# Kernel tuning notes

Measured on AMD Instinct MI355X. Metric: run time of the kernel, lower is better.

Reference implementation:

```python
import jax, jax.numpy as jnp
import numpy as np

RANK = 16
ALPHA = 32.0
LORA_SCALE = ALPHA / RANK  # 2.0


def setup_inputs() -> dict:
    key = jax.random.key(0)
    ks = jax.random.split(key, 7)
    B_, S, D_IN, D_OUT = 4, 2048, 4096, 4096
    x = jax.random.normal(ks[0], (B_, S, D_IN), dtype=jnp.float32)
    qweight = jax.random.randint(ks[1], (D_OUT, D_IN), 0, 16, dtype=jnp.int32)
    w_min = jax.random.normal(ks[2], (D_OUT, 1), dtype=jnp.float32) * 0.1
    # row scale ~ (max-min)/15 of typical weights; keep positive
    w_scale = jax.random.uniform(ks[3], (D_OUT, 1), dtype=jnp.float32, minval=1e-3, maxval=0.02)
    bias = jax.random.normal(ks[4], (D_OUT,), dtype=jnp.float32) * 0.02
    A = jax.random.normal(ks[5], (RANK, D_IN), dtype=jnp.float32) * 0.02
    # module inits B to zeros; use small randn so the LoRA branch is exercised
    Bm = jax.random.normal(ks[6], (D_OUT, RANK), dtype=jnp.float32) * 0.02
    return {"x": x, "qweight": qweight, "w_min": w_min, "w_scale": w_scale,
            "bias": bias, "A": A, "B": Bm}


def reference(x, qweight, w_min, w_scale, bias, A, B):
    # Row-wise 4-bit dequant: W[o,i] = q[o,i]*scale[o] + min[o]
    base_weight = qweight.astype(jnp.float32) * w_scale + w_min  # [O, I]
    base_out = jnp.einsum('bsi,oi->bso', x, base_weight) + bias   # [B, S, O]
    # LoRA: (x @ A^T) @ B^T * (alpha/rank); dropout p=0 is identity
    lora_out = jnp.einsum('bsr,or->bso', jnp.einsum('bsi,ri->bsr', x, A), B) * LORA_SCALE
    return base_out + lora_out
```

## Files before the change

kernel.cpp:

```cpp
#include <hip/hip_runtime.h>
#include <hip/hip_bf16.h>

typedef unsigned short u16;
typedef unsigned int u32;
typedef __bf16 bf16x8 __attribute__((ext_vector_type(8)));
typedef float f32x4 __attribute__((ext_vector_type(4)));
typedef u16 u16x4 __attribute__((ext_vector_type(4)));
typedef u16 u16x8 __attribute__((ext_vector_type(8)));

#define D_IN 4096
#define D_OUT 4096
#define M_TOT 8192
#define RANK_ 16

#define BM 256
#define BN 256
#define BK 64
#define NT (D_IN / BK)
#define OPB 2

__device__ __forceinline__ u16 f2bf(float f) {
    union { float f; u32 u; } v; v.f = f;
    u32 u = v.u;
    u32 r = (u + 0x7FFFu + ((u >> 16) & 1u)) >> 16;
    return (u16)r;
}

__global__ __launch_bounds__(256) void dequant_fold_kernel(
        const int* __restrict__ q, const float* __restrict__ wmin,
        const float* __restrict__ wscale, const float* __restrict__ A,
        const float* __restrict__ Bm, u16* __restrict__ Wb) {
    const int K = D_IN;
    int o0 = blockIdx.x * OPB;
    float s0 = wscale[o0], s1 = wscale[o0 + 1];
    float m0 = wmin[o0],   m1 = wmin[o0 + 1];
    float Br0[RANK_], Br1[RANK_];
    #pragma unroll
    for (int r = 0; r < RANK_; ++r) {
        Br0[r] = 2.0f * Bm[(size_t)o0 * RANK_ + r];
        Br1[r] = 2.0f * Bm[(size_t)(o0 + 1) * RANK_ + r];
    }
    for (int i4 = threadIdx.x; i4 < K / 4; i4 += 256) {
        int i = i4 * 4;
        int4 q0 = *(const int4*)(q + (size_t)o0 * K + i);
        int4 q1 = *(const int4*)(q + (size_t)(o0 + 1) * K + i);
        float v00 = (float)q0.x * s0 + m0, v01 = (float)q0.y * s0 + m0;
        float v02 = (float)q0.z * s0 + m0, v03 = (float)q0.w * s0 + m0;
        float v10 = (float)q1.x * s1 + m1, v11 = (float)q1.y * s1 + m1;
        float v12 = (float)q1.z * s1 + m1, v13 = (float)q1.w * s1 + m1;
        #pragma unroll
        for (int r = 0; r < RANK_; ++r) {
            float4 av = *(const float4*)(A + (size_t)r * K + i);
            v00 += Br0[r] * av.x; v01 += Br0[r] * av.y;
            v02 += Br0[r] * av.z; v03 += Br0[r] * av.w;
            v10 += Br1[r] * av.x; v11 += Br1[r] * av.y;
            v12 += Br1[r] * av.z; v13 += Br1[r] * av.w;
        }
        u16x4 o0v, o1v;
        o0v.x = f2bf(v00); o0v.y = f2bf(v01); o0v.z = f2bf(v02); o0v.w = f2bf(v03);
        o1v.x = f2bf(v10); o1v.y = f2bf(v11); o1v.z = f2bf(v12); o1v.w = f2bf(v13);
        *(u16x4*)(Wb + (size_t)o0 * K + i) = o0v;
        *(u16x4*)(Wb + (size_t)(o0 + 1) * K + i) = o1v;
    }
}

__global__ void xcast_kernel(const float* __restrict__ x, u16* __restrict__ xb) {
    size_t i = (size_t)blockIdx.x * blockDim.x + threadIdx.x;
    const float4* p = (const float4*)x + i * 2;
    float4 a = p[0];
    float4 b = p[1];
    u16x8 o;
    o[0] = f2bf(a.x); o[1] = f2bf(a.y); o[2] = f2bf(a.z); o[3] = f2bf(a.w);
    o[4] = f2bf(b.x); o[5] = f2bf(b.y); o[6] = f2bf(b.z); o[7] = f2bf(b.w);
    *(u16x8*)(xb + i * 8) = o;
}


#define STAGE_R(sarr, larr, base, kt) do { _Pragma("unroll") \
    for (int j_ = 0; j_ < 2; ++j_) \
        __builtin_amdgcn_global_load_lds( \
            (__attribute__((address_space(1))) u32*)(sarr[j_] + (kt) * 64), \
            (__attribute__((address_space(3))) u32*)(smem + (base) + larr[j_]), \
            16, 0, 0); } while (0)

#define MFMA(d, va, vb) d = __builtin_amdgcn_mfma_f32_16x16x32_bf16(va, vb, d, 0, 0, 0)

__global__ __launch_bounds__(512, 2) void gemm_bt_kernel(const u16* __restrict__ Xb,
                                                         const u16* __restrict__ Wb,
                                                         const float* __restrict__ bias,
                                                         float* __restrict__ out) {
    extern __shared__ __align__(16) char smem[];
    const int K = D_IN, N = D_OUT;

    int bid = blockIdx.x;
    int swz = (bid & 7) * 64 + (bid >> 3);
    int tM = swz >> 4;
    int tN = swz & 15;

    int t = threadIdx.x;
    int lane = t & 63;
    int wave = t >> 6;
    int wm = wave >> 2;
    int wn = wave & 3;
    int lr = lane & 15;
    int hi = lane >> 4;
    int l7 = lane & 7;

    int xs0 = ((0 * 4 + hi) ^ l7) << 4;
    int xs1 = ((1 * 4 + hi) ^ l7) << 4;
    int aRow = (wm * 128 + lr) * 128;
    int bRow = (wn * 64 + lr) * 128;

    const u16 *srcA03[2], *srcA47[2], *srcB01[2], *srcB23[2];
    int ldsA03[2], ldsA47[2], ldsB01[2], ldsB23[2];
    #pragma unroll
    for (int j = 0; j < 2; ++j) {
        int idx = j * 512 + t;
        int rl = idx >> 3, slot = idx & 7;
        int rA = (rl & 63) + ((rl >> 6) << 7);
        int rB = (rl & 31) + ((rl >> 5) << 6);
        int r = rA;
        ldsA03[j] = r * 128 + slot * 16;
        srcA03[j] = Xb + (size_t)(tM * 256 + r) * K + ((slot ^ (r & 7)) << 3);
        r = rA + 64;
        ldsA47[j] = r * 128 + slot * 16;
        srcA47[j] = Xb + (size_t)(tM * 256 + r) * K + ((slot ^ (r & 7)) << 3);
        r = rB;
        ldsB01[j] = r * 128 + slot * 16;
        srcB01[j] = Wb + (size_t)(tN * 256 + r) * K + ((slot ^ (r & 7)) << 3);
        r = rB + 32;
        ldsB23[j] = r * 128 + slot * 16;
        srcB23[j] = Wb + (size_t)(tN * 256 + r) * K + ((slot ^ (r & 7)) << 3);
    }

    f32x4 acc[8][4];
    #pragma unroll
    for (int i = 0; i < 8; ++i)
        #pragma unroll
        for (int j = 0; j < 4; ++j)
            acc[i][j] = (f32x4){0.f, 0.f, 0.f, 0.f};

    STAGE_R(srcA03, ldsA03, 0, 0);     STAGE_R(srcA47, ldsA47, 0, 0);
    STAGE_R(srcB01, ldsB01, 65536, 0); STAGE_R(srcB23, ldsB23, 65536, 0);
    STAGE_R(srcA03, ldsA03, 32768, 1); STAGE_R(srcA47, ldsA47, 32768, 1);
    STAGE_R(srcB01, ldsB01, 98304, 1); STAGE_R(srcB23, ldsB23, 98304, 1);
    asm volatile("s_waitcnt vmcnt(8)" ::: "memory");
    __builtin_amdgcn_s_barrier();

    bf16x8 a[4][2], b23[2][2], b01[2][2];
    #pragma unroll
    for (int nf = 0; nf < 2; ++nf) {
        b01[nf][0] = *(const bf16x8*)(smem + 65536 + bRow + nf * 2048 + xs0);
        b01[nf][1] = *(const bf16x8*)(smem + 65536 + bRow + nf * 2048 + xs1);
    }

    for (int tt = 0; tt < NT; ++tt) {
        int pA = (tt & 1) * 32768;
        int pB = 65536 + (tt & 1) * 32768;
        int pBn = 65536 + ((~tt) & 1) * 32768;
        bool pre = (tt + 2 < NT);

        #pragma unroll
        for (int mf = 0; mf < 4; ++mf) {
            a[mf][0] = *(const bf16x8*)(smem + pA + aRow + mf * 2048 + xs0);
            a[mf][1] = *(const bf16x8*)(smem + pA + aRow + mf * 2048 + xs1);
        }
        asm volatile("s_waitcnt lgkmcnt(4)" ::: "memory");
        __builtin_amdgcn_s_barrier();
        asm volatile("s_waitcnt lgkmcnt(0)");
        __builtin_amdgcn_s_setprio(1);
        #pragma unroll
        for (int mf = 0; mf < 4; ++mf)
            #pragma unroll
            for (int nf = 0; nf < 2; ++nf) {
                MFMA(acc[mf][nf], a[mf][0], b01[nf][0]);
                MFMA(acc[mf][nf], a[mf][1], b01[nf][1]);
            }
        __builtin_amdgcn_s_setprio(0);
        __builtin_amdgcn_s_barrier();

        #pragma unroll
        for (int nf = 0; nf < 2; ++nf) {
            b23[nf][0] = *(const bf16x8*)(smem + pB + bRow + (nf + 2) * 2048 + xs0);
            b23[nf][1] = *(const bf16x8*)(smem + pB + bRow + (nf + 2) * 2048 + xs1);
        }
        if (pre) {
            STAGE_R(srcA03, ldsA03, pA, tt + 2);
            STAGE_R(srcB01, ldsB01, pB, tt + 2);
        }
        __builtin_amdgcn_s_barrier();
        asm volatile("s_waitcnt lgkmcnt(0)");
        __builtin_amdgcn_s_setprio(1);
        #pragma unroll
        for (int mf = 0; mf < 4; ++mf)
            #pragma unroll
            for (int nf = 0; nf < 2; ++nf) {
                MFMA(acc[mf][nf + 2], a[mf][0], b23[nf][0]);
                MFMA(acc[mf][nf + 2], a[mf][1], b23[nf][1]);
            }
        __builtin_amdgcn_s_setprio(0);
        __builtin_amdgcn_s_barrier();

        #pragma unroll
        for (int mf = 0; mf < 4; ++mf) {
            a[mf][0] = *(const bf16x8*)(smem + pA + aRow + (mf + 4) * 2048 + xs0);
            a[mf][1] = *(const bf16x8*)(smem + pA + aRow + (mf + 4) * 2048 + xs1);
        }
        if (pre) { STAGE_R(srcB23, ldsB23, pB, tt + 2); }
        asm volatile("s_waitcnt lgkmcnt(4)" ::: "memory");
        __builtin_amdgcn_s_barrier();
        asm volatile("s_waitcnt lgkmcnt(0)");
        __builtin_amdgcn_s_setprio(1);
        #pragma unroll
        for (int mf = 0; mf < 4; ++mf)
            #pragma unroll
            for (int nf = 0; nf < 2; ++nf) {
                MFMA(acc[mf + 4][nf], a[mf][0], b01[nf][0]);
                MFMA(acc[mf + 4][nf], a[mf][1], b01[nf][1]);
            }
        __builtin_amdgcn_s_setprio(0);
        __builtin_amdgcn_s_barrier();

        if (pre) { STAGE_R(srcA47, ldsA47, pA, tt + 2); }
        if (tt < NT - 2) { asm volatile("s_waitcnt vmcnt(8)" ::: "memory"); }
        else             { asm volatile("s_waitcnt vmcnt(0)" ::: "memory"); }
        __builtin_amdgcn_s_barrier();
        if (tt + 1 < NT) {
            #pragma unroll
            for (int nf = 0; nf < 2; ++nf) {
                b01[nf][0] = *(const bf16x8*)(smem + pBn + bRow + nf * 2048 + xs0);
                b01[nf][1] = *(const bf16x8*)(smem + pBn + bRow + nf * 2048 + xs1);
            }
        }
        __builtin_amdgcn_s_setprio(1);
        #pragma unroll
        for (int mf = 0; mf < 4; ++mf)
            #pragma unroll
            for (int nf = 0; nf < 2; ++nf) {
                MFMA(acc[mf + 4][nf + 2], a[mf][0], b23[nf][0]);
                MFMA(acc[mf + 4][nf + 2], a[mf][1], b23[nf][1]);
            }
        __builtin_amdgcn_s_setprio(0);
        __builtin_amdgcn_s_barrier();
    }

    #pragma unroll
    for (int nf = 0; nf < 4; ++nf) {
        int gn = tN * 256 + wn * 64 + nf * 16 + lr;
        float bs = bias[gn];
        #pragma unroll
        for (int mf = 0; mf < 8; ++mf) {
            #pragma unroll
            for (int r = 0; r < 4; ++r) {
                int gm = tM * 256 + wm * 128 + mf * 16 + hi * 4 + r;
                out[(size_t)gm * N + gn] = acc[mf][nf][r] + bs;
            }
        }
    }
}

extern "C" void kernel_launch(void* const* d_in, const int* in_sizes, int n_in,
                              void* d_out, int out_size, void* d_ws, size_t ws_size,
                              hipStream_t stream) {
    (void)in_sizes; (void)n_in; (void)out_size; (void)ws_size;
    const float* x      = (const float*)d_in[0];
    const int*   qw     = (const int*)d_in[1];
    const float* wmin   = (const float*)d_in[2];
    const float* wscale = (const float*)d_in[3];
    const float* bias   = (const float*)d_in[4];
    const float* A      = (const float*)d_in[5];
    const float* Bm     = (const float*)d_in[6];
    float* out = (float*)d_out;

    u16* Wb = (u16*)d_ws;
    u16* Xb = Wb + (size_t)D_OUT * D_IN;

    dequant_fold_kernel<<<D_OUT / OPB, 256, 0, stream>>>(qw, wmin, wscale, A, Bm, Wb);
    xcast_kernel<<<(M_TOT * D_IN) / (256 * 8), 256, 0, stream>>>(x, Xb);
    gemm_bt_kernel<<<(M_TOT / BM) * (D_OUT / BN), 512, 131072, stream>>>(Xb, Wb, bias, out);
}
```

Measured before the change: 302.6 us.

## Switch GEMM inner loop from 16x16x32 to 32x32x16 bf16 MFMA tiles

```diff
diff --git a/kernel.cpp b/kernel.cpp
--- a/kernel.cpp
+++ b/kernel.cpp
@@ -5,6 +5,7 @@
 typedef unsigned int u32;
 typedef __bf16 bf16x8 __attribute__((ext_vector_type(8)));
 typedef float f32x4 __attribute__((ext_vector_type(4)));
+typedef float f32x16 __attribute__((ext_vector_type(16)));
 typedef u16 u16x4 __attribute__((ext_vector_type(4)));
 typedef u16 u16x8 __attribute__((ext_vector_type(8)));
 
@@ -83,7 +84,7 @@
             (__attribute__((address_space(3))) u32*)(smem + (base) + larr[j_]), \
             16, 0, 0); } while (0)
 
-#define MFMA(d, va, vb) d = __builtin_amdgcn_mfma_f32_16x16x32_bf16(va, vb, d, 0, 0, 0)
+#define MFMA32(d, va, vb) d = __builtin_amdgcn_mfma_f32_32x32x16_bf16(va, vb, d, 0, 0, 0)
 
 __global__ __launch_bounds__(512, 2) void gemm_bt_kernel(const u16* __restrict__ Xb,
                                                          const u16* __restrict__ Wb,
@@ -102,14 +103,15 @@
     int wave = t >> 6;
     int wm = wave >> 2;
     int wn = wave & 3;
-    int lr = lane & 15;
-    int hi = lane >> 4;
+    int l31 = lane & 31;
+    int hi5 = lane >> 5;
     int l7 = lane & 7;
 
-    int xs0 = ((0 * 4 + hi) ^ l7) << 4;
-    int xs1 = ((1 * 4 + hi) ^ l7) << 4;
-    int aRow = (wm * 128 + lr) * 128;
-    int bRow = (wn * 64 + lr) * 128;
+    int xsl[4];
+    #pragma unroll
+    for (int ks = 0; ks < 4; ++ks) xsl[ks] = ((2 * ks + hi5) ^ l7) << 4;
+    int aRowB = (wm * 128 + l31) * 128;
+    int bRowB = (wn * 64 + l31) * 128;
 
     const u16 *srcA03[2], *srcA47[2], *srcB01[2], *srcB23[2];
     int ldsA03[2], ldsA47[2], ldsB01[2], ldsB23[2];
@@ -133,12 +135,13 @@
         srcB23[j] = Wb + (size_t)(tN * 256 + r) * K + ((slot ^ (r & 7)) << 3);
     }
 
-    f32x4 acc[8][4];
-    #pragma unroll
-    for (int i = 0; i < 8; ++i)
-        #pragma unroll
-        for (int j = 0; j < 4; ++j)
-            acc[i][j] = (f32x4){0.f, 0.f, 0.f, 0.f};
+    f32x16 acc[4][2];
+    #pragma unroll
+    for (int i = 0; i < 4; ++i)
+        #pragma unroll
+        for (int j = 0; j < 2; ++j)
+            acc[i][j] = (f32x16){0.f,0.f,0.f,0.f,0.f,0.f,0.f,0.f,
+                                 0.f,0.f,0.f,0.f,0.f,0.f,0.f,0.f};
 
     STAGE_R(srcA03, ldsA03, 0, 0);     STAGE_R(srcA47, ldsA47, 0, 0);
     STAGE_R(srcB01, ldsB01, 65536, 0); STAGE_R(srcB23, ldsB23, 65536, 0);
@@ -147,12 +150,10 @@
     asm volatile("s_waitcnt vmcnt(8)" ::: "memory");
     __builtin_amdgcn_s_barrier();
 
-    bf16x8 a[4][2], b23[2][2], b01[2][2];
-    #pragma unroll
-    for (int nf = 0; nf < 2; ++nf) {
-        b01[nf][0] = *(const bf16x8*)(smem + 65536 + bRow + nf * 2048 + xs0);
-        b01[nf][1] = *(const bf16x8*)(smem + 65536 + bRow + nf * 2048 + xs1);
-    }
+    bf16x8 a[2][4], bnf0[4], bnf1[4];
+    #pragma unroll
+    for (int ks = 0; ks < 4; ++ks)
+        bnf0[ks] = *(const bf16x8*)(smem + 65536 + bRowB + xsl[ks]);
 
     for (int tt = 0; tt < NT; ++tt) {
         int pA = (tt & 1) * 32768;
@@ -161,29 +162,25 @@
         bool pre = (tt + 2 < NT);
 
         #pragma unroll
-        for (int mf = 0; mf < 4; ++mf) {
-            a[mf][0] = *(const bf16x8*)(smem + pA + aRow + mf * 2048 + xs0);
-            a[mf][1] = *(const bf16x8*)(smem + pA + aRow + mf * 2048 + xs1);
-        }
-        asm volatile("s_waitcnt lgkmcnt(4)" ::: "memory");
+        for (int m = 0; m < 2; ++m)
+            #pragma unroll
+            for (int ks = 0; ks < 4; ++ks)
+                a[m][ks] = *(const bf16x8*)(smem + pA + aRowB + m * 4096 + xsl[ks]);
+        asm volatile("s_waitcnt lgkmcnt(8)" ::: "memory");
         __builtin_amdgcn_s_barrier();
         asm volatile("s_waitcnt lgkmcnt(0)");
         __builtin_amdgcn_s_setprio(1);
         #pragma unroll
-        for (int mf = 0; mf < 4; ++mf)
-            #pragma unroll
-            for (int nf = 0; nf < 2; ++nf) {
-                MFMA(acc[mf][nf], a[mf][0], b01[nf][0]);
-                MFMA(acc[mf][nf], a[mf][1], b01[nf][1]);
-            }
-        __builtin_amdgcn_s_setprio(0);
-        __builtin_amdgcn_s_barrier();
-
-        #pragma unroll
-        for (int nf = 0; nf < 2; ++nf) {
-            b23[nf][0] = *(const bf16x8*)(smem + pB + bRow + (nf + 2) * 2048 + xs0);
-            b23[nf][1] = *(const bf16x8*)(smem + pB + bRow + (nf + 2) * 2048 + xs1);
-        }
+        for (int m = 0; m < 2; ++m)
+            #pragma unroll
+            for (int ks = 0; ks < 4; ++ks)
+                MFMA32(acc[m][0], a[m][ks], bnf0[ks]);
+        __builtin_amdgcn_s_setprio(0);
+        __builtin_amdgcn_s_barrier();
+
+        #pragma unroll
+        for (int ks = 0; ks < 4; ++ks)
+            bnf1[ks] = *(const bf16x8*)(smem + pB + bRowB + 4096 + xsl[ks]);
         if (pre) {
             STAGE_R(srcA03, ldsA03, pA, tt + 2);
             STAGE_R(srcB01, ldsB01, pB, tt + 2);
@@ -192,32 +189,27 @@
         asm volatile("s_waitcnt lgkmcnt(0)");
         __builtin_amdgcn_s_setprio(1);
         #pragma unroll
-        for (int mf = 0; mf < 4; ++mf)
-            #pragma unroll
-            for (int nf = 0; nf < 2; ++nf) {
-                MFMA(acc[mf][nf + 2], a[mf][0], b23[nf][0]);
-                MFMA(acc[mf][nf + 2], a[mf][1], b23[nf][1]);
-            }
-        __builtin_amdgcn_s_setprio(0);
-        __builtin_amdgcn_s_barrier();
-
-        #pragma unroll
-        for (int mf = 0; mf < 4; ++mf) {
-            a[mf][0] = *(const bf16x8*)(smem + pA + aRow + (mf + 4) * 2048 + xs0);
-            a[mf][1] = *(const bf16x8*)(smem + pA + aRow + (mf + 4) * 2048 + xs1);
-        }
+        for (int m = 0; m < 2; ++m)
+            #pragma unroll
+            for (int ks = 0; ks < 4; ++ks)
+                MFMA32(acc[m][1], a[m][ks], bnf1[ks]);
+        __builtin_amdgcn_s_setprio(0);
+        __builtin_amdgcn_s_barrier();
+
+        #pragma unroll
+        for (int m = 0; m < 2; ++m)
+            #pragma unroll
+            for (int ks = 0; ks < 4; ++ks)
+                a[m][ks] = *(const bf16x8*)(smem + pA + aRowB + (m + 2) * 4096 + xsl[ks]);
         if (pre) { STAGE_R(srcB23, ldsB23, pB, tt + 2); }
-        asm volatile("s_waitcnt lgkmcnt(4)" ::: "memory");
         __builtin_amdgcn_s_barrier();
         asm volatile("s_waitcnt lgkmcnt(0)");
         __builtin_amdgcn_s_setprio(1);
         #pragma unroll
-        for (int mf = 0; mf < 4; ++mf)
-            #pragma unroll
-            for (int nf = 0; nf < 2; ++nf) {
-                MFMA(acc[mf + 4][nf], a[mf][0], b01[nf][0]);
-                MFMA(acc[mf + 4][nf], a[mf][1], b01[nf][1]);
-            }
+        for (int m = 0; m < 2; ++m)
+            #pragma unroll
+            for (int ks = 0; ks < 4; ++ks)
+                MFMA32(acc[m + 2][0], a[m][ks], bnf0[ks]);
         __builtin_amdgcn_s_setprio(0);
         __builtin_amdgcn_s_barrier();
 
@@ -227,33 +219,30 @@
         __builtin_amdgcn_s_barrier();
         if (tt + 1 < NT) {
             #pragma unroll
-            for (int nf = 0; nf < 2; ++nf) {
-                b01[nf][0] = *(const bf16x8*)(smem + pBn + bRow + nf * 2048 + xs0);
-                b01[nf][1] = *(const bf16x8*)(smem + pBn + bRow + nf * 2048 + xs1);
-            }
-        }
-        __builtin_amdgcn_s_setprio(1);
-        #pragma unroll
-        for (int mf = 0; mf < 4; ++mf)
-            #pragma unroll
-            for (int nf = 0; nf < 2; ++nf) {
-                MFMA(acc[mf + 4][nf + 2], a[mf][0], b23[nf][0]);
-                MFMA(acc[mf + 4][nf + 2], a[mf][1], b23[nf][1]);
-            }
-        __builtin_amdgcn_s_setprio(0);
-        __builtin_amdgcn_s_barrier();
-    }
-
-    #pragma unroll
-    for (int nf = 0; nf < 4; ++nf) {
-        int gn = tN * 256 + wn * 64 + nf * 16 + lr;
+            for (int ks = 0; ks < 4; ++ks)
+                bnf0[ks] = *(const bf16x8*)(smem + pBn + bRowB + xsl[ks]);
+        }
+        __builtin_amdgcn_s_setprio(1);
+        #pragma unroll
+        for (int m = 0; m < 2; ++m)
+            #pragma unroll
+            for (int ks = 0; ks < 4; ++ks)
+                MFMA32(acc[m + 2][1], a[m][ks], bnf1[ks]);
+        __builtin_amdgcn_s_setprio(0);
+        __builtin_amdgcn_s_barrier();
+    }
+
+    #pragma unroll
+    for (int nf = 0; nf < 2; ++nf) {
+        int gn = tN * 256 + wn * 64 + nf * 32 + l31;
         float bs = bias[gn];
         #pragma unroll
-        for (int mf = 0; mf < 8; ++mf) {
-            #pragma unroll
-            for (int r = 0; r < 4; ++r) {
-                int gm = tM * 256 + wm * 128 + mf * 16 + hi * 4 + r;
-                out[(size_t)gm * N + gn] = acc[mf][nf][r] + bs;
+        for (int m = 0; m < 4; ++m) {
+            #pragma unroll
+            for (int reg = 0; reg < 16; ++reg) {
+                int gm = tM * 256 + wm * 128 + m * 32
+                       + (reg & 3) + ((reg >> 2) << 3) + (hi5 << 2);
+                out[(size_t)gm * N + gn] = acc[m][nf][reg] + bs;
             }
         }
     }
```

After: 329.4 us. 1.09x slower.
